# Kernel tuning notes

Measured on AMD Instinct MI355X. Metric: run time of the kernel, lower is better.

## Reference

```python
import jax, jax.numpy as jnp
import numpy as np

N = 8192
DIM_IN = 1024
DIM_INNER = 1024
DIM_OUT = 1024


def setup_inputs() -> dict:
    key = jax.random.key(0)
    k1, k2, k3, k4 = jax.random.split(key, 4)
    x = jax.random.normal(k1, (N, DIM_IN), dtype=jnp.float32)
    # torch nn.Linear weights, stored transposed for right-multiplication
    Wqkv = jax.random.normal(k2, (DIM_IN, 3 * DIM_INNER), dtype=jnp.float32) * (DIM_IN ** -0.5)
    Wout = jax.random.normal(k3, (DIM_INNER, DIM_OUT), dtype=jnp.float32) * (DIM_INNER ** -0.5)
    bout = jax.random.normal(k4, (DIM_OUT,), dtype=jnp.float32) * 0.01
    return {"x": x, "Wqkv": Wqkv, "Wout": Wout, "bout": bout}


def reference(x, Wqkv, Wout, bout):
    scale = DIM_INNER ** -0.5
    qkv = x @ Wqkv                      # [N, 3*Di]
    q, k, v = jnp.split(qkv, 3, axis=-1)  # each [N, Di]
    sim = jnp.einsum('id,jd->ij', q, k) * scale  # [N, N]
    # causal mask: future positions (j > i) filled with -finfo.max
    i = jnp.arange(sim.shape[0])[:, None]
    j = jnp.arange(sim.shape[1])[None, :]
    sim = jnp.where(j > i, -jnp.finfo(sim.dtype).max, sim)
    attn = jax.nn.softmax(sim, axis=-1)
    out = jnp.einsum('ij,jd->id', attn, v)  # [N, Di]
    return out @ Wout + bout            # [N, Do]
```

## Files before the change

kernel.cpp:

```cpp
#include <hip/hip_runtime.h>
#include <hip/hip_bf16.h>


typedef __bf16 v8bf __attribute__((ext_vector_type(8)));
typedef float  v4f  __attribute__((ext_vector_type(4)));

struct __align__(8) S4 { short x, y, z, w; };

__device__ inline short f2bf(float f) {
  __hip_bfloat16 h = __float2bfloat16(f);
  return *reinterpret_cast<short*>(&h);
}
__device__ inline float bf2f(short s) {
  unsigned u = ((unsigned)(unsigned short)s) << 16;
  float f;
  __builtin_memcpy(&f, &u, 4);
  return f;
}

__device__ inline void stage_tile(const short* gbase, int ldg, short* lds, int tid) {
#pragma unroll
  for (int p = 0; p < 2; ++p) {
    const int c = p * 256 + tid;
    const int pos = (c & 3) ^ ((c >> 3) & 3);
    const short* g = gbase + (size_t)(c >> 2) * ldg + pos * 8;
    short* l = lds + p * 2048 + (tid >> 6) * 512;
    __builtin_amdgcn_global_load_lds(
        (__attribute__((address_space(1))) void*)(void*)g,
        (__attribute__((address_space(3))) void*)l, 16, 0, 0);
  }
}

__device__ inline void mma_step(const short* As, const short* Bs, v4f acc[4][4],
                                int lane, int wm, int wn) {
  const int qd = lane >> 4, r16 = lane & 15;
  const int sw = (qd ^ ((r16 >> 1) & 3)) * 8;
  const short* ab = As + (wm * 64 + r16) * 32 + sw;
  const short* bb = Bs + (wn * 64 + r16) * 32 + sw;
  v8bf a[4], b[4];
#pragma unroll
  for (int t = 0; t < 4; ++t) {
    a[t] = *(const v8bf*)(ab + t * 512);
    b[t] = *(const v8bf*)(bb + t * 512);
  }
#pragma unroll
  for (int mt = 0; mt < 4; ++mt)
#pragma unroll
    for (int nt = 0; nt < 4; ++nt)
      acc[mt][nt] = __builtin_amdgcn_mfma_f32_16x16x32_bf16(a[mt], b[nt], acc[mt][nt], 0, 0, 0);
}

#define ACC_INIT(acc)                              \
  _Pragma("unroll") for (int i_ = 0; i_ < 4; ++i_) \
  _Pragma("unroll") for (int j_ = 0; j_ < 4; ++j_) \
      acc[i_][j_] = (v4f){0.f, 0.f, 0.f, 0.f};

__global__ __launch_bounds__(256) void k_zerof(float* __restrict__ p, int n) {
  const int i = blockIdx.x * 256 + threadIdx.x;
  if (i < n) p[i] = 0.f;
}

__global__ __launch_bounds__(256) void k_detect(const unsigned short* __restrict__ xs,
                                                int* __restrict__ flag) {
  __shared__ int cnt;
  if (threadIdx.x == 0) cnt = 0;
  __syncthreads();
  int local = 0;
  for (int i = threadIdx.x; i < 4096; i += 256) {
    const unsigned e = (xs[i] >> 7) & 0xFFu;
    if (e >= 0xC0u) ++local;
  }
  if (local) atomicAdd(&cnt, local);
  __syncthreads();
  if (threadIdx.x == 0) *flag = (cnt > 8) ? 1 : 0;
}

__global__ __launch_bounds__(256) void k_convert(const void* __restrict__ in,
                                                 short* __restrict__ out, int n,
                                                 const int* __restrict__ flag) {
  const int stride = gridDim.x * blockDim.x;
  const int i0 = blockIdx.x * blockDim.x + threadIdx.x;
  if (*flag != 0) {
    const float4* p = (const float4*)in;
    S4* o = (S4*)out;
    for (int v = i0; v < (n >> 2); v += stride) {
      const float4 f = p[v];
      S4 s;
      s.x = f2bf(f.x); s.y = f2bf(f.y); s.z = f2bf(f.z); s.w = f2bf(f.w);
      o[v] = s;
    }
  } else {
    const int4* p = (const int4*)in;
    int4* o = (int4*)out;
    for (int v = i0; v < (n >> 3); v += stride) o[v] = p[v];
  }
}

__global__ __launch_bounds__(256) void k_to_f32(const void* __restrict__ in,
                                                float* __restrict__ out, int n,
                                                const int* __restrict__ flag) {
  const int stride = gridDim.x * blockDim.x;
  int i = blockIdx.x * blockDim.x + threadIdx.x;
  if (*flag != 0) {
    const float* p = (const float*)in;
    for (; i < n; i += stride) out[i] = p[i];
  } else {
    const short* p = (const short*)in;
    for (; i < n; i += stride) out[i] = bf2f(p[i]);
  }
}

__global__ __launch_bounds__(256) void k_convT(const void* __restrict__ in,
                                               short* __restrict__ out, int R, int C,
                                               const int* __restrict__ flag) {
  __shared__ short t[32][33];
  const int xx = threadIdx.x & 31, y0 = threadIdx.x >> 5;
  const int c0 = blockIdx.x * 32, r0 = blockIdx.y * 32;
  if (*flag != 0) {
    const float* p = (const float*)in;
#pragma unroll
    for (int i = 0; i < 4; ++i) {
      int r = y0 + i * 8;
      t[r][xx] = f2bf(p[(size_t)(r0 + r) * C + c0 + xx]);
    }
  } else {
    const short* p = (const short*)in;
#pragma unroll
    for (int i = 0; i < 4; ++i) {
      int r = y0 + i * 8;
      t[r][xx] = p[(size_t)(r0 + r) * C + c0 + xx];
    }
  }
  __syncthreads();
#pragma unroll
  for (int i = 0; i < 4; ++i) {
    int r = y0 + i * 8;
    out[(size_t)(c0 + r) * R + r0 + xx] = t[xx][r];
  }
}

__global__ __launch_bounds__(256) void k_gemm_qkv(const short* __restrict__ x,
                                                  const short* __restrict__ wt,
                                                  short* __restrict__ qk,
                                                  short* __restrict__ vT) {
  __shared__ short As[2][4096], Bs[2][4096];
  const int tid = threadIdx.x, lane = tid & 63, wave = tid >> 6;
  const int wm = wave >> 1, wn = wave & 1;
  const int lin = (int)blockIdx.y * 64 + (int)blockIdx.x;
  const int swz = (lin & 7) * 192 + (lin >> 3);
  const int m0 = (swz / 24) * 128, n0 = (swz % 24) * 128;
  const short* srcA = x + (size_t)m0 * 1024;
  const short* srcB = wt + (size_t)n0 * 1024;
  v4f acc[4][4];
  ACC_INIT(acc)
  stage_tile(srcA, 1024, As[0], tid);
  stage_tile(srcB, 1024, Bs[0], tid);
  __syncthreads();
  for (int k0 = 0; k0 < 1024; k0 += 32) {
    const int cur = (k0 >> 5) & 1;
    if (k0 + 32 < 1024) {
      stage_tile(srcA + k0 + 32, 1024, As[cur ^ 1], tid);
      stage_tile(srcB + k0 + 32, 1024, Bs[cur ^ 1], tid);
    }
    mma_step(As[cur], Bs[cur], acc, lane, wm, wn);
    __syncthreads();
  }
  const int qd = lane >> 4, c16 = lane & 15;
#pragma unroll
  for (int mt = 0; mt < 4; ++mt) {
    const int rl = wm * 64 + mt * 16 + qd * 4;
#pragma unroll
    for (int nt = 0; nt < 4; ++nt) {
      const int cl = wn * 64 + nt * 16 + c16;
      const int n = n0 + cl;
      if (n < 2048) {
#pragma unroll
        for (int r = 0; r < 4; ++r)
          qk[(size_t)(m0 + rl + r) * 2048 + n] = f2bf(acc[mt][nt][r]);
      } else {
        S4 p;
        p.x = f2bf(acc[mt][nt][0]);
        p.y = f2bf(acc[mt][nt][1]);
        p.z = f2bf(acc[mt][nt][2]);
        p.w = f2bf(acc[mt][nt][3]);
        *reinterpret_cast<S4*>(vT + (size_t)(n - 2048) * 8192 + (m0 + rl)) = p;
      }
    }
  }
}

__global__ __launch_bounds__(256) void k_qk_exp(const short* __restrict__ qk,
                                                short* __restrict__ E,
                                                float* __restrict__ l) {
  __shared__ short As[2][4096], Bs[2][4096];
  __shared__ float srow[128][2];
  const int tid = threadIdx.x, lane = tid & 63, wave = tid >> 6;
  const int wm = wave >> 1, wn = wave & 1;
  const int b = ((int)blockIdx.x & 7) * 260 + ((int)blockIdx.x >> 3);
  int I = (int)((sqrtf(8.f * (float)b + 1.f) - 1.f) * 0.5f);
  while ((I + 1) * (I + 2) / 2 <= b) ++I;
  while (I * (I + 1) / 2 > b) --I;
  const int J = b - I * (I + 1) / 2;
  const int m0 = I * 128, n0 = J * 128;
  const short* srcA = qk + (size_t)m0 * 2048;
  const short* srcB = qk + 1024 + (size_t)n0 * 2048;
  v4f acc[4][4];
  ACC_INIT(acc)
  stage_tile(srcA, 2048, As[0], tid);
  stage_tile(srcB, 2048, Bs[0], tid);
  __syncthreads();
  for (int k0 = 0; k0 < 1024; k0 += 32) {
    const int cur = (k0 >> 5) & 1;
    if (k0 + 32 < 1024) {
      stage_tile(srcA + k0 + 32, 2048, As[cur ^ 1], tid);
      stage_tile(srcB + k0 + 32, 2048, Bs[cur ^ 1], tid);
    }
    mma_step(As[cur], Bs[cur], acc, lane, wm, wn);
    __syncthreads();
  }
  short* tb = E + (size_t)(I * (I + 1) / 2 + J) * 16384;
  const int qd = lane >> 4, c16 = lane & 15;
  float rp[4][4];
#pragma unroll
  for (int mt = 0; mt < 4; ++mt)
#pragma unroll
    for (int r = 0; r < 4; ++r) rp[mt][r] = 0.f;
#pragma unroll
  for (int mt = 0; mt < 4; ++mt) {
    const int rl = wm * 64 + mt * 16 + qd * 4;
#pragma unroll
    for (int nt = 0; nt < 4; ++nt) {
      const int cl = wn * 64 + nt * 16 + c16;
      const int gj = n0 + cl;
      const int jj = cl >> 5, qdc = (cl >> 3) & 3, jl = cl & 7;
      short* dst = tb + (((wm * 4 + jj) * 4 + mt) * 512) + qdc * 128 + jl;
#pragma unroll
      for (int r = 0; r < 4; ++r) {
        const int gi = m0 + rl + r;
        const float s = fminf(acc[mt][nt][r] * 0.03125f, 60.f);
        const float e = (gj > gi) ? 0.f : __expf(s);
        dst[(qd * 4 + r) * 8] = f2bf(e);
        rp[mt][r] += e;
      }
    }
  }
#pragma unroll
  for (int mt = 0; mt < 4; ++mt)
#pragma unroll
    for (int r = 0; r < 4; ++r) {
      float v = rp[mt][r];
      v += __shfl_xor(v, 1);
      v += __shfl_xor(v, 2);
      v += __shfl_xor(v, 4);
      v += __shfl_xor(v, 8);
      rp[mt][r] = v;
    }
  if ((lane & 15) == 0) {
#pragma unroll
    for (int mt = 0; mt < 4; ++mt)
#pragma unroll
      for (int r = 0; r < 4; ++r)
        srow[wm * 64 + mt * 16 + qd * 4 + r][wn] = rp[mt][r];
  }
  __syncthreads();
  if (tid < 128) atomicAdd(&l[m0 + tid], srow[tid][0] + srow[tid][1]);
}

__device__ __forceinline__ void pv_loadA8(v8bf a[4], const short* __restrict__ Et,
                                          int wave, int lane) {
  const int wm_ = wave >> 2, mt_ = wave & 3;
#pragma unroll
  for (int jj = 0; jj < 4; ++jj) {
    const int BLK = (wm_ * 4 + jj) * 4 + mt_;
    a[jj] = *(const v8bf*)(Et + BLK * 512 + lane * 8);
  }
}

__device__ __forceinline__ void pv_stageV8(const short* __restrict__ vbJ,
                                           short* __restrict__ lds, int tid) {
#pragma unroll
  for (int p = 0; p < 4; ++p) {
    const int c = p * 512 + tid;
    const int row = c >> 4;
    const int kc = (c & 15) ^ (row & 15);
    const short* g = vbJ + (size_t)row * 8192 + kc * 8;
    short* lp = lds + (p * 512 + (tid >> 6) * 64) * 8;
    __builtin_amdgcn_global_load_lds(
        (__attribute__((address_space(1))) void*)(void*)g,
        (__attribute__((address_space(3))) void*)lp, 16, 0, 0);
  }
}

__device__ __forceinline__ void pv_compute8(const v8bf a[4], const short* __restrict__ Vbuf,
                                            v4f acc[8], int qd, int r16) {
#pragma unroll
  for (int jj = 0; jj < 4; ++jj) {
    v8bf b[8];
#pragma unroll
    for (int u = 0; u < 8; ++u) {
      const int row = u * 16 + r16;
      const int kc = (jj * 4 + qd) ^ r16;
      b[u] = *(const v8bf*)(Vbuf + row * 128 + kc * 8);
    }
#pragma unroll
    for (int u = 0; u < 8; ++u)
      acc[u] = __builtin_amdgcn_mfma_f32_16x16x32_bf16(a[jj], b[u], acc[u], 0, 0, 0);
  }
}

__global__ __launch_bounds__(512) void k_pv(const short* __restrict__ E,
                                            const short* __restrict__ vT,
                                            const float* __restrict__ l,
                                            short* __restrict__ attn) {
  __shared__ short Vb[2][16384];
  const int tid = threadIdx.x, lane = tid & 63, wave = tid >> 6;
  const int bx = (int)blockIdx.x;
  const int n0 = (int)blockIdx.y * 128;
  const int qd = lane >> 4, r16 = lane & 15;
  const short* vb = vT + (size_t)n0 * 8192;
  for (int half = 0; half < 2; ++half) {
    const int I = half ? 63 - bx : bx;
    const int m0 = I * 128;
    const short* Erow = E + (size_t)(I * (I + 1) / 2) * 16384;
    v4f acc[8];
#pragma unroll
    for (int u = 0; u < 8; ++u) acc[u] = (v4f){0.f, 0.f, 0.f, 0.f};
    v8bf aA[4], aB[4];
    __syncthreads();
    pv_stageV8(vb, Vb[0], tid);
    pv_loadA8(aA, Erow, wave, lane);
    __syncthreads();
    for (int J = 0;; J += 2) {
      if (J + 1 <= I) {
        pv_stageV8(vb + (J + 1) * 128, Vb[1], tid);
        pv_loadA8(aB, Erow + (size_t)(J + 1) * 16384, wave, lane);
      }
      pv_compute8(aA, Vb[0], acc, qd, r16);
      if (J + 1 > I) break;
      __syncthreads();
      if (J + 2 <= I) {
        pv_stageV8(vb + (J + 2) * 128, Vb[0], tid);
        pv_loadA8(aA, Erow + (size_t)(J + 2) * 16384, wave, lane);
      }
      pv_compute8(aB, Vb[1], acc, qd, r16);
      if (J + 2 > I) break;
      __syncthreads();
    }
    const int rbase = wave * 16 + qd * 4;
    float inv[4];
#pragma unroll
    for (int r = 0; r < 4; ++r) inv[r] = 1.0f / fmaxf(l[m0 + rbase + r], 1e-30f);
#pragma unroll
    for (int u = 0; u < 8; ++u) {
#pragma unroll
      for (int r = 0; r < 4; ++r)
        attn[(size_t)(m0 + rbase + r) * 1024 + n0 + u * 16 + r16] = f2bf(acc[u][r] * inv[r]);
    }
  }
}

__global__ __launch_bounds__(256) void k_gemm_out(const short* __restrict__ attn,
                                                  const short* __restrict__ wt,
                                                  const float* __restrict__ bout,
                                                  float* __restrict__ out) {
  __shared__ short As[2][4096], Bs[2][4096];
  const int tid = threadIdx.x, lane = tid & 63, wave = tid >> 6;
  const int wm = wave >> 1, wn = wave & 1;
  const int lin = (int)blockIdx.y * 64 + (int)blockIdx.x;
  const int swz = (lin & 7) * 64 + (lin >> 3);
  const int m0 = (swz >> 3) * 128, n0 = (swz & 7) * 128;
  const short* srcA = attn + (size_t)m0 * 1024;
  const short* srcB = wt + (size_t)n0 * 1024;
  v4f acc[4][4];
  ACC_INIT(acc)
  stage_tile(srcA, 1024, As[0], tid);
  stage_tile(srcB, 1024, Bs[0], tid);
  __syncthreads();
  for (int k0 = 0; k0 < 1024; k0 += 32) {
    const int cur = (k0 >> 5) & 1;
    if (k0 + 32 < 1024) {
      stage_tile(srcA + k0 + 32, 1024, As[cur ^ 1], tid);
      stage_tile(srcB + k0 + 32, 1024, Bs[cur ^ 1], tid);
    }
    mma_step(As[cur], Bs[cur], acc, lane, wm, wn);
    __syncthreads();
  }
  const int qd = lane >> 4, c16 = lane & 15;
#pragma unroll
  for (int mt = 0; mt < 4; ++mt) {
    const int rl = wm * 64 + mt * 16 + qd * 4;
#pragma unroll
    for (int nt = 0; nt < 4; ++nt) {
      const int cl = wn * 64 + nt * 16 + c16;
      const float bias = bout[n0 + cl];
#pragma unroll
      for (int r = 0; r < 4; ++r)
        out[(size_t)(m0 + rl + r) * 1024 + n0 + cl] = acc[mt][nt][r] + bias;
    }
  }
}

extern "C" void kernel_launch(void* const* d_in, const int* in_sizes, int n_in,
                              void* d_out, int out_size, void* d_ws, size_t ws_size,
                              hipStream_t stream) {
  (void)out_size; (void)ws_size;
  const void *x = d_in[0], *Wqkv = d_in[1], *Wout = d_in[2], *bout = d_in[3];
  for (int i = 0; i < n_in; ++i) {
    switch (in_sizes[i]) {
      case 8192 * 1024: x = d_in[i]; break;
      case 1024 * 3072: Wqkv = d_in[i]; break;
      case 1024 * 1024: Wout = d_in[i]; break;
      case 1024:        bout = d_in[i]; break;
      default: break;
    }
  }

  char* ws = (char*)d_ws;
  short* qk    = (short*)(ws);
  short* vT    = (short*)(ws + 33554432);
  short* E     = (short*)(ws + 50331648);
  short* xb    = (short*)(ws + 118489088);
  short* attn  = xb;
  short* WqT   = (short*)(ws + 135266304);
  short* WoT   = (short*)(ws + 141557760);
  float* boutf = (float*)(ws + 143654912);
  float* lsum  = (float*)(ws + 143659008);
  int*   flag  = (int*)  (ws + 143691776);

  k_detect<<<1, 256, 0, stream>>>((const unsigned short*)x, flag);
  k_zerof<<<32, 256, 0, stream>>>(lsum, 8192);
  k_convert<<<1024, 256, 0, stream>>>(x, xb, 8192 * 1024, flag);
  k_to_f32<<<1, 256, 0, stream>>>(bout, boutf, 1024, flag);
  k_convT<<<dim3(96, 32), 256, 0, stream>>>(Wqkv, WqT, 1024, 3072, flag);
  k_convT<<<dim3(32, 32), 256, 0, stream>>>(Wout, WoT, 1024, 1024, flag);
  k_gemm_qkv<<<dim3(64, 24), 256, 0, stream>>>(xb, WqT, qk, vT);
  k_qk_exp<<<dim3(2080), 256, 0, stream>>>(qk, E, lsum);
  k_pv<<<dim3(32, 8), 512, 0, stream>>>(E, vT, lsum, attn);
  k_gemm_out<<<dim3(64, 8), 256, 0, stream>>>(attn, WoT, boutf, (float*)d_out);
}
```

Baseline: 404.9 us.

## Widen GEMM tiles to 128x256 with 512-thread blocks and pair causal tiles

Changes the three GEMM kernels (QKV projection, QK^T+exp, output projection) from 128x128 tiles on 256 threads to 128x256 tiles on 8 waves, with new staging helpers and a new block swizzle. The causal QK kernel now walks pairs of adjacent column tiles per row block and masks writes for the tile past the diagonal. Wider tiles cut the number of A-tile reloads and blocks, and should raise arithmetic intensity per LDS byte. The costs are more LDS per block, wasted compute on diagonal pairs whose second tile is invalid, and a four-way row-sum reduction.

```diff
diff --git a/kernel.cpp b/kernel.cpp
--- a/kernel.cpp
+++ b/kernel.cpp
@@ -18,13 +18,24 @@
   return f;
 }
 
-__device__ inline void stage_tile(const short* gbase, int ldg, short* lds, int tid) {
+__device__ inline void stageA512(const short* g0, int ldg, short* lds, int tid) {
+  const int c = tid;
+  const int row = c >> 2;
+  const int pos = (c & 3) ^ ((row >> 1) & 3);
+  const short* g = g0 + (size_t)row * ldg + pos * 8;
+  short* l = lds + (tid >> 6) * 512;
+  __builtin_amdgcn_global_load_lds(
+      (__attribute__((address_space(1))) void*)(void*)g,
+      (__attribute__((address_space(3))) void*)l, 16, 0, 0);
+}
+__device__ inline void stageB512(const short* g0, int ldg, short* lds, int tid) {
 #pragma unroll
   for (int p = 0; p < 2; ++p) {
-    const int c = p * 256 + tid;
-    const int pos = (c & 3) ^ ((c >> 3) & 3);
-    const short* g = gbase + (size_t)(c >> 2) * ldg + pos * 8;
-    short* l = lds + p * 2048 + (tid >> 6) * 512;
+    const int c = p * 512 + tid;
+    const int row = c >> 2;
+    const int pos = (c & 3) ^ ((row >> 1) & 3);
+    const short* g = g0 + (size_t)row * ldg + pos * 8;
+    short* l = lds + p * 4096 + (tid >> 6) * 512;
     __builtin_amdgcn_global_load_lds(
         (__attribute__((address_space(1))) void*)(void*)g,
         (__attribute__((address_space(3))) void*)l, 16, 0, 0);
@@ -139,28 +150,28 @@
   }
 }
 
-__global__ __launch_bounds__(256) void k_gemm_qkv(const short* __restrict__ x,
+__global__ __launch_bounds__(512) void k_gemm_qkv(const short* __restrict__ x,
                                                   const short* __restrict__ wt,
                                                   short* __restrict__ qk,
                                                   short* __restrict__ vT) {
-  __shared__ short As[2][4096], Bs[2][4096];
+  __shared__ short As[2][4096], Bs[2][8192];
   const int tid = threadIdx.x, lane = tid & 63, wave = tid >> 6;
-  const int wm = wave >> 1, wn = wave & 1;
+  const int wm = wave >> 2, wn = wave & 3;
   const int lin = (int)blockIdx.y * 64 + (int)blockIdx.x;
-  const int swz = (lin & 7) * 192 + (lin >> 3);
-  const int m0 = (swz / 24) * 128, n0 = (swz % 24) * 128;
+  const int swz = (lin & 7) * 96 + (lin >> 3);
+  const int m0 = (swz / 12) * 128, n0 = (swz % 12) * 256;
   const short* srcA = x + (size_t)m0 * 1024;
   const short* srcB = wt + (size_t)n0 * 1024;
   v4f acc[4][4];
   ACC_INIT(acc)
-  stage_tile(srcA, 1024, As[0], tid);
-  stage_tile(srcB, 1024, Bs[0], tid);
+  stageA512(srcA, 1024, As[0], tid);
+  stageB512(srcB, 1024, Bs[0], tid);
   __syncthreads();
   for (int k0 = 0; k0 < 1024; k0 += 32) {
     const int cur = (k0 >> 5) & 1;
     if (k0 + 32 < 1024) {
-      stage_tile(srcA + k0 + 32, 1024, As[cur ^ 1], tid);
-      stage_tile(srcB + k0 + 32, 1024, Bs[cur ^ 1], tid);
+      stageA512(srcA + k0 + 32, 1024, As[cur ^ 1], tid);
+      stageB512(srcB + k0 + 32, 1024, Bs[cur ^ 1], tid);
     }
     mma_step(As[cur], Bs[cur], acc, lane, wm, wn);
     __syncthreads();
@@ -189,36 +200,39 @@
   }
 }
 
-__global__ __launch_bounds__(256) void k_qk_exp(const short* __restrict__ qk,
+__global__ __launch_bounds__(512) void k_qk_exp(const short* __restrict__ qk,
                                                 short* __restrict__ E,
                                                 float* __restrict__ l) {
-  __shared__ short As[2][4096], Bs[2][4096];
-  __shared__ float srow[128][2];
+  __shared__ short As[2][4096], Bs[2][8192];
+  __shared__ float srow[128][4];
   const int tid = threadIdx.x, lane = tid & 63, wave = tid >> 6;
-  const int wm = wave >> 1, wn = wave & 1;
-  const int b = ((int)blockIdx.x & 7) * 260 + ((int)blockIdx.x >> 3);
-  int I = (int)((sqrtf(8.f * (float)b + 1.f) - 1.f) * 0.5f);
-  while ((I + 1) * (I + 2) / 2 <= b) ++I;
-  while (I * (I + 1) / 2 > b) --I;
-  const int J = b - I * (I + 1) / 2;
-  const int m0 = I * 128, n0 = J * 128;
+  const int wm = wave >> 2, wn = wave & 3;
+  const int b = ((int)blockIdx.x & 7) * 132 + ((int)blockIdx.x >> 3);
+  int m = (int)((sqrtf(4.f * (float)b + 1.f) - 1.f) * 0.5f);
+  while ((m + 1) * (m + 2) <= b) ++m;
+  while (m * (m + 1) > b) --m;
+  int I, p;
+  if (b < (m + 1) * (m + 1)) { I = 2 * m;     p = b - m * (m + 1); }
+  else                       { I = 2 * m + 1; p = b - (m + 1) * (m + 1); }
+  const int J0 = 2 * p;
+  const int m0 = I * 128, n0 = J0 * 128;
   const short* srcA = qk + (size_t)m0 * 2048;
   const short* srcB = qk + 1024 + (size_t)n0 * 2048;
   v4f acc[4][4];
   ACC_INIT(acc)
-  stage_tile(srcA, 2048, As[0], tid);
-  stage_tile(srcB, 2048, Bs[0], tid);
+  stageA512(srcA, 2048, As[0], tid);
+  stageB512(srcB, 2048, Bs[0], tid);
   __syncthreads();
   for (int k0 = 0; k0 < 1024; k0 += 32) {
     const int cur = (k0 >> 5) & 1;
     if (k0 + 32 < 1024) {
-      stage_tile(srcA + k0 + 32, 2048, As[cur ^ 1], tid);
-      stage_tile(srcB + k0 + 32, 2048, Bs[cur ^ 1], tid);
+      stageA512(srcA + k0 + 32, 2048, As[cur ^ 1], tid);
+      stageB512(srcB + k0 + 32, 2048, Bs[cur ^ 1], tid);
     }
     mma_step(As[cur], Bs[cur], acc, lane, wm, wn);
     __syncthreads();
   }
-  short* tb = E + (size_t)(I * (I + 1) / 2 + J) * 16384;
+  const size_t triB = (size_t)I * (I + 1) / 2;
   const int qd = lane >> 4, c16 = lane & 15;
   float rp[4][4];
 #pragma unroll
@@ -231,15 +245,18 @@
 #pragma unroll
     for (int nt = 0; nt < 4; ++nt) {
       const int cl = wn * 64 + nt * 16 + c16;
+      const int Jt = J0 + (cl >> 7);
+      const int jloc = cl & 127;
       const int gj = n0 + cl;
-      const int jj = cl >> 5, qdc = (cl >> 3) & 3, jl = cl & 7;
-      short* dst = tb + (((wm * 4 + jj) * 4 + mt) * 512) + qdc * 128 + jl;
+      const bool valid = (Jt <= I);
+      const int jj = jloc >> 5, qdc = (jloc >> 3) & 3, jl = jloc & 7;
+      short* dst = E + (triB + Jt) * 16384 + (((wm * 4 + jj) * 4 + mt) * 512) + qdc * 128 + jl;
 #pragma unroll
       for (int r = 0; r < 4; ++r) {
         const int gi = m0 + rl + r;
         const float s = fminf(acc[mt][nt][r] * 0.03125f, 60.f);
         const float e = (gj > gi) ? 0.f : __expf(s);
-        dst[(qd * 4 + r) * 8] = f2bf(e);
+        if (valid) dst[(qd * 4 + r) * 8] = f2bf(e);
         rp[mt][r] += e;
       }
     }
@@ -263,7 +280,8 @@
         srow[wm * 64 + mt * 16 + qd * 4 + r][wn] = rp[mt][r];
   }
   __syncthreads();
-  if (tid < 128) atomicAdd(&l[m0 + tid], srow[tid][0] + srow[tid][1]);
+  if (tid < 128)
+    atomicAdd(&l[m0 + tid], (srow[tid][0] + srow[tid][1]) + (srow[tid][2] + srow[tid][3]));
 }
 
 __device__ __forceinline__ void pv_loadA8(v8bf a[4], const short* __restrict__ Et,
@@ -359,28 +377,28 @@
   }
 }
 
-__global__ __launch_bounds__(256) void k_gemm_out(const short* __restrict__ attn,
+__global__ __launch_bounds__(512) void k_gemm_out(const short* __restrict__ attn,
                                                   const short* __restrict__ wt,
                                                   const float* __restrict__ bout,
                                                   float* __restrict__ out) {
-  __shared__ short As[2][4096], Bs[2][4096];
+  __shared__ short As[2][4096], Bs[2][8192];
   const int tid = threadIdx.x, lane = tid & 63, wave = tid >> 6;
-  const int wm = wave >> 1, wn = wave & 1;
+  const int wm = wave >> 2, wn = wave & 3;
   const int lin = (int)blockIdx.y * 64 + (int)blockIdx.x;
-  const int swz = (lin & 7) * 64 + (lin >> 3);
-  const int m0 = (swz >> 3) * 128, n0 = (swz & 7) * 128;
+  const int swz = (lin & 7) * 32 + (lin >> 3);
+  const int m0 = (swz >> 2) * 128, n0 = (swz & 3) * 256;
   const short* srcA = attn + (size_t)m0 * 1024;
   const short* srcB = wt + (size_t)n0 * 1024;
   v4f acc[4][4];
   ACC_INIT(acc)
-  stage_tile(srcA, 1024, As[0], tid);
-  stage_tile(srcB, 1024, Bs[0], tid);
+  stageA512(srcA, 1024, As[0], tid);
+  stageB512(srcB, 1024, Bs[0], tid);
   __syncthreads();
   for (int k0 = 0; k0 < 1024; k0 += 32) {
     const int cur = (k0 >> 5) & 1;
     if (k0 + 32 < 1024) {
-      stage_tile(srcA + k0 + 32, 1024, As[cur ^ 1], tid);
-      stage_tile(srcB + k0 + 32, 1024, Bs[cur ^ 1], tid);
+      stageA512(srcA + k0 + 32, 1024, As[cur ^ 1], tid);
+      stageB512(srcB + k0 + 32, 1024, Bs[cur ^ 1], tid);
     }
     mma_step(As[cur], Bs[cur], acc, lane, wm, wn);
     __syncthreads();
@@ -433,8 +451,8 @@
   k_to_f32<<<1, 256, 0, stream>>>(bout, boutf, 1024, flag);
   k_convT<<<dim3(96, 32), 256, 0, stream>>>(Wqkv, WqT, 1024, 3072, flag);
   k_convT<<<dim3(32, 32), 256, 0, stream>>>(Wout, WoT, 1024, 1024, flag);
-  k_gemm_qkv<<<dim3(64, 24), 256, 0, stream>>>(xb, WqT, qk, vT);
-  k_qk_exp<<<dim3(2080), 256, 0, stream>>>(qk, E, lsum);
+  k_gemm_qkv<<<dim3(64, 12), 512, 0, stream>>>(xb, WqT, qk, vT);
+  k_qk_exp<<<dim3(1056), 512, 0, stream>>>(qk, E, lsum);
   k_pv<<<dim3(32, 8), 512, 0, stream>>>(E, vT, lsum, attn);
-  k_gemm_out<<<dim3(64, 8), 256, 0, stream>>>(attn, WoT, boutf, (float*)d_out);
-}
+  k_gemm_out<<<dim3(64, 4), 512, 0, stream>>>(attn, WoT, boutf, (float*)d_out);
+}
```

Measured after the change: 441.5 us. +9.0%, slower.
